# Optimization experiments

Hardware: AMD Instinct MI355X
Metric: run time of the kernel (lower is better)

## Reference

```python
import jax, jax.numpy as jnp
import numpy as np

INPUT_DIM = 512
N_CLASSES = 100
N_SUBNETS = 20
HIDDEN = 32
WS1 = INPUT_DIM * HIDDEN   # 16384
BS1 = HIDDEN               # 32
WS2 = HIDDEN * N_CLASSES   # 3200
BS2 = N_CLASSES            # 100
TOTAL = WS1 + BS1 + WS2 + BS2  # 19716
LN_EPS = 1e-5


def _layernorm(v, g, b):
    mu = jnp.mean(v, axis=-1, keepdims=True)
    var = jnp.mean(jnp.square(v - mu), axis=-1, keepdims=True)
    return (v - mu) * jax.lax.rsqrt(var + LN_EPS) * g + b


def setup_inputs() -> dict:
    key = jax.random.key(0)
    ks = jax.random.split(key, 12)
    def lin(k, fan_in, shape):
        bound = 1.0 / np.sqrt(fan_in)
        return jax.random.uniform(k, shape, jnp.float32, -bound, bound)
    return {
        "x": jax.random.normal(ks[0], (32768, INPUT_DIM), jnp.float32),
        "W_h1": lin(ks[1], INPUT_DIM, (128, INPUT_DIM)),
        "b_h1": lin(ks[2], INPUT_DIM, (128,)),
        "g1": jnp.ones((128,), jnp.float32),
        "be1": jnp.zeros((128,), jnp.float32),
        "W_h2": lin(ks[3], 128, (256, 128)),
        "b_h2": lin(ks[4], 128, (256,)),
        "g2": jnp.ones((256,), jnp.float32),
        "be2": jnp.zeros((256,), jnp.float32),
        "W_h3": lin(ks[5], 256, (N_SUBNETS * TOTAL, 256)),
        "b_h3": lin(ks[6], 256, (N_SUBNETS * TOTAL,)),
        "ens_w": jnp.full((N_SUBNETS,), 1.0 / N_SUBNETS, jnp.float32),
    }


def reference(x, W_h1, b_h1, g1, be1, W_h2, b_h2, g2, be2, W_h3, b_h3, ens_w):
    # context from support set (= x itself): (1, input_dim)
    context = jnp.mean(x, axis=0, keepdims=True)
    # hypernet MLP (eval mode: dropout = identity)
    h = jax.nn.relu(_layernorm(context @ W_h1.T + b_h1, g1, be1))
    h = jax.nn.relu(_layernorm(h @ W_h2.T + b_h2, g2, be2))
    all_params = (h @ W_h3.T + b_h3).reshape(N_SUBNETS, TOTAL)
    # split generated params (same layout as torch .view)
    W1 = all_params[:, :WS1].reshape(N_SUBNETS, HIDDEN, INPUT_DIM)       # (S,H,I)
    b1 = all_params[:, WS1:WS1 + BS1]                                     # (S,H)
    W2 = all_params[:, WS1 + BS1:WS1 + BS1 + WS2].reshape(N_SUBNETS, N_CLASSES, HIDDEN)  # (S,C,H)
    b2 = all_params[:, WS1 + BS1 + WS2:]                                  # (S,C)
    # batched per-subnet 2-layer nets (dropout p=0.2 is identity in eval)
    hh = jax.nn.relu(jnp.einsum('bi,shi->sbh', x, W1) + b1[:, None, :])   # (S,B,H)
    logits = jnp.einsum('sbh,sch->sbc', hh, W2) + b2[:, None, :]          # (S,B,C)
    w = jax.nn.softmax(ens_w)                                             # (S,)
    return jnp.einsum('s,sbc->bc', w, logits)                             # (B,C)
```

## Files before the change

kernel.cpp:

```cpp
#include <hip/hip_runtime.h>
#include <hip/hip_bf16.h>

#define BATCH   32768
#define DIM     512
#define H1N     128
#define H2N     256
#define NSUB    20
#define HID     32
#define NCLS    100
#define NHID    640
#define TOTALP  19716
#define NPAR    394320
#define WS1P    16384
#define WS1B1   16416
#define WS2END  19616

#define OFF_PART 0
#define OFF_H    262144
#define OFF_W    262400
#define OFF_B1   262432
#define OFF_B2R  263072
#define OFF_W1B  265072
#define OFF_W2B  428912

typedef __attribute__((ext_vector_type(8))) short short8;
typedef __attribute__((ext_vector_type(4))) float f32x4;

static __device__ inline unsigned short f2bf(float f) {
    __hip_bfloat16 h = __float2bfloat16(f);
    return *reinterpret_cast<unsigned short*>(&h);
}

static __device__ __forceinline__ void gload16(const void* g, void* l) {
    __builtin_amdgcn_global_load_lds(
        (const __attribute__((address_space(1))) void*)g,
        (__attribute__((address_space(3))) void*)l, 16, 0, 0);
}

__global__ __launch_bounds__(256) void k1_colsum(const float* __restrict__ x,
                                                 float* __restrict__ F) {
    __shared__ float sP[DIM];
    int t = threadIdx.x, bid = blockIdx.x;
    int par = t >> 7;
    int c4 = (t & 127) * 4;
    const float* xb = x + (size_t)bid * 64 * DIM;
    float4 acc = make_float4(0.f, 0.f, 0.f, 0.f);
    #pragma unroll 8
    for (int i = 0; i < 32; ++i) {
        int r = 2 * i + par;
        float4 v = *(const float4*)(xb + r * DIM + c4);
        acc.x += v.x; acc.y += v.y; acc.z += v.z; acc.w += v.w;
    }
    if (par == 0) *(float4*)(sP + c4) = acc;
    __syncthreads();
    if (par == 1) {
        float4 p = *(const float4*)(sP + c4);
        p.x += acc.x; p.y += acc.y; p.z += acc.z; p.w += acc.w;
        *(float4*)(F + OFF_PART + bid * DIM + c4) = p;
    }
}

__global__ __launch_bounds__(256) void k2_hyper(
    const float* __restrict__ Wh1, const float* __restrict__ bh1,
    const float* __restrict__ g1,  const float* __restrict__ be1,
    const float* __restrict__ Wh2, const float* __restrict__ bh2,
    const float* __restrict__ g2,  const float* __restrict__ be2,
    const float* __restrict__ ensw, float* __restrict__ F)
{
    __shared__ __align__(16) float sctx[DIM];
    __shared__ __align__(16) float sP2[DIM];
    __shared__ __align__(16) float sh1[H1N];
    __shared__ __align__(16) float sh2[H2N];
    int t = threadIdx.x;

    {
        int c4 = (t & 127) * 4;
        int half = t >> 7;
        float4 a = make_float4(0.f, 0.f, 0.f, 0.f);
        #pragma unroll 8
        for (int b = half * 256; b < half * 256 + 256; ++b) {
            float4 v = *(const float4*)(F + OFF_PART + b * DIM + c4);
            a.x += v.x; a.y += v.y; a.z += v.z; a.w += v.w;
        }
        if (half == 0) *(float4*)(sP2 + c4) = a;
        __syncthreads();
        if (half == 1) {
            float4 o = *(const float4*)(sP2 + c4);
            o.x = (o.x + a.x) * (1.0f / BATCH);
            o.y = (o.y + a.y) * (1.0f / BATCH);
            o.z = (o.z + a.z) * (1.0f / BATCH);
            o.w = (o.w + a.w) * (1.0f / BATCH);
            *(float4*)(sctx + c4) = o;
        }
        __syncthreads();
    }

    if (t < H1N) {
        float v = bh1[t];
        const float4* w = (const float4*)(Wh1 + t * DIM);
        for (int k = 0; k < DIM / 4; ++k) {
            float4 ww = w[k]; float4 c = *(const float4*)(sctx + k * 4);
            v += ww.x * c.x + ww.y * c.y + ww.z * c.z + ww.w * c.w;
        }
        sh1[t] = v;
    }
    __syncthreads();
    {
        float mu = 0.f;
        for (int k = 0; k < H1N; ++k) mu += sh1[k];
        mu *= (1.0f / H1N);
        float var = 0.f;
        for (int k = 0; k < H1N; ++k) { float d = sh1[k] - mu; var += d * d; }
        var *= (1.0f / H1N);
        float inv = rsqrtf(var + 1e-5f);
        __syncthreads();
        if (t < H1N) {
            float v = (sh1[t] - mu) * inv * g1[t] + be1[t];
            sh1[t] = fmaxf(v, 0.f);
        }
        __syncthreads();
    }

    {
        float v = bh2[t];
        const float4* w = (const float4*)(Wh2 + t * H1N);
        for (int k = 0; k < H1N / 4; ++k) {
            float4 ww = w[k]; float4 c = *(const float4*)(sh1 + k * 4);
            v += ww.x * c.x + ww.y * c.y + ww.z * c.z + ww.w * c.w;
        }
        sh2[t] = v;
    }
    __syncthreads();
    {
        float mu = 0.f;
        for (int k = 0; k < H2N; ++k) mu += sh2[k];
        mu *= (1.0f / H2N);
        float var = 0.f;
        for (int k = 0; k < H2N; ++k) { float d = sh2[k] - mu; var += d * d; }
        var *= (1.0f / H2N);
        float inv = rsqrtf(var + 1e-5f);
        float v = (sh2[t] - mu) * inv * g2[t] + be2[t];
        F[OFF_H + t] = fmaxf(v, 0.f);
    }

    if (t == 0) {
        float m = -1e30f;
        for (int s = 0; s < NSUB; ++s) m = fmaxf(m, ensw[s]);
        float sum = 0.f, e[NSUB];
        for (int s = 0; s < NSUB; ++s) { e[s] = __expf(ensw[s] - m); sum += e[s]; }
        for (int s = 0; s < NSUB; ++s) F[OFF_W + s] = e[s] / sum;
    }
}

static __device__ __forceinline__ void k3_pack(float* F, int row, float val) {
    __hip_bfloat16* W1B = (__hip_bfloat16*)(F + OFF_W1B);
    __hip_bfloat16* W2B = (__hip_bfloat16*)(F + OFF_W2B);
    int s = row / TOTALP;
    int r = row - s * TOTALP;
    if (r < WS1P) {
        int hh = r >> 9, k = r & 511;
        W1B[(s * HID + hh) * DIM + k] = __float2bfloat16(val);
    } else if (r < WS1B1) {
        F[OFF_B1 + s * HID + (r - WS1P)] = val;
    } else if (r < WS2END) {
        int q = r - WS1B1; int c = q >> 5, hh = q & 31;
        float ws = F[OFF_W + s];
        W2B[c * NHID + s * HID + hh] = __float2bfloat16(ws * val);
    } else {
        F[OFF_B2R + s * NCLS + (r - WS2END)] = val;
    }
}

__global__ __launch_bounds__(256) void k3_gemv(
    const float* __restrict__ Wh3, const float* __restrict__ bh3, float* __restrict__ F)
{
    int t = threadIdx.x;
    int wid = t >> 6, lane = t & 63;
    int row0 = blockIdx.x * 8 + wid * 2;
    const float4 h = *(const float4*)(F + OFF_H + lane * 4);
    const float4 w0 = *(const float4*)(Wh3 + (size_t)row0 * 256 + lane * 4);
    const float4 w1 = *(const float4*)(Wh3 + (size_t)(row0 + 1) * 256 + lane * 4);
    float d0 = w0.x * h.x + w0.y * h.y + w0.z * h.z + w0.w * h.w;
    float d1 = w1.x * h.x + w1.y * h.y + w1.z * h.z + w1.w * h.w;
    #pragma unroll
    for (int off = 32; off; off >>= 1) {
        d0 += __shfl_down(d0, off);
        d1 += __shfl_down(d1, off);
    }
    if (lane == 0) {
        k3_pack(F, row0,     d0 + bh3[row0]);
        k3_pack(F, row0 + 1, d1 + bh3[row0 + 1]);
    }
}

__global__ __launch_bounds__(256) void gemm_fused(
    const float* __restrict__ x, const __hip_bfloat16* __restrict__ W1B,
    const __hip_bfloat16* __restrict__ W2B, const float* __restrict__ F,
    float* __restrict__ out)
{
    __shared__ __align__(16) unsigned char sB[2][128 * 128];
    __shared__ __align__(16) unsigned char sP[64 * 256];
    const int t = threadIdx.x;
    int bid = blockIdx.x;
    const int cpx = gridDim.x >> 3;
    bid = (bid & 7) * cpx + (bid >> 3);
    const int Row0 = bid * 64;
    const int wid = t >> 6, lane = t & 63;
    const int l16 = lane & 15, lq = lane >> 4;

    f32x4 acc1[8], acc2[8];
    #pragma unroll
    for (int fn = 0; fn < 8; ++fn) acc2[fn] = (f32x4){0.f, 0.f, 0.f, 0.f};

    auto stageW1 = [&](int n1, int kc, int b) {
        #pragma unroll
        for (int i = 0; i < 4; ++i) {
            int cidx = wid * 4 + i;
            int ul = cidx * 64 + lane;
            int row = ul >> 3, u = ul & 7;
            gload16(W1B + (size_t)(n1 * 128 + row) * 512 + kc + ((u ^ (row & 7)) << 3),
                    &sB[b][cidx * 1024]);
        }
    };
    auto stageW2 = [&](int n1, int h, int b) {
        #pragma unroll
        for (int i = 0; i < 4; ++i) {
            int cidx = wid * 4 + i;
            int ul = cidx * 64 + lane;
            int row = ul >> 3, u = ul & 7;
            gload16(W2B + (size_t)row * NHID + n1 * 128 + h * 64 + ((u ^ (row & 7)) << 3),
                    &sB[b][cidx * 1024]);
        }
    };

    stageW1(0, 0, 0);

    short8 afr[16];
    {
        const float* xrow = x + (size_t)(Row0 + wid * 16 + l16) * 512;
        #pragma unroll
        for (int i = 0; i < 16; ++i) {
            int k0 = (i >> 1) * 64 + (i & 1) * 32 + lq * 8;
            float4 a = *(const float4*)(xrow + k0);
            float4 b = *(const float4*)(xrow + k0 + 4);
            unsigned int p[4];
            p[0] = (unsigned)f2bf(a.x) | ((unsigned)f2bf(a.y) << 16);
            p[1] = (unsigned)f2bf(a.z) | ((unsigned)f2bf(a.w) << 16);
            p[2] = (unsigned)f2bf(b.x) | ((unsigned)f2bf(b.y) << 16);
            p[3] = (unsigned)f2bf(b.z) | ((unsigned)f2bf(b.w) << 16);
            afr[i] = *(short8*)p;
        }
    }
    asm volatile("s_waitcnt vmcnt(0)" ::: "memory");
    __builtin_amdgcn_s_barrier();

    auto comp1 = [&](int st, int b) {
        #pragma unroll
        for (int kk = 0; kk < 2; ++kk) {
            int u = kk * 4 + lq;
            short8 af = afr[st * 2 + kk];
            short8 bfv[8];
            #pragma unroll
            for (int fn = 0; fn < 8; ++fn) {
                int rw = fn * 16 + l16;
                bfv[fn] = *(const short8*)(&sB[b][rw * 128 + ((u ^ (rw & 7)) << 4)]);
            }
            #pragma unroll
            for (int fn = 0; fn < 8; ++fn)
                acc1[fn] = __builtin_amdgcn_mfma_f32_16x16x32_bf16(
                    af, bfv[fn], acc1[fn], 0, 0, 0);
        }
    };
    auto comp2 = [&](int h, int b) {
        #pragma unroll
        for (int kk = 0; kk < 2; ++kk) {
            int u = kk * 4 + lq;
            int punit = (h * 2 + kk) * 4 + lq;
            int arow = wid * 16 + l16;
            short8 af = *(const short8*)(&sP[arow * 256 + ((punit ^ (arow & 7)) << 4)]);
            short8 bfv[8];
            #pragma unroll
            for (int fn = 0; fn < 8; ++fn) {
                int rw = fn * 16 + l16;
                bfv[fn] = *(const short8*)(&sB[b][rw * 128 + ((u ^ (rw & 7)) << 4)]);
            }
            #pragma unroll
            for (int fn = 0; fn < 8; ++fn)
                acc2[fn] = __builtin_amdgcn_mfma_f32_16x16x32_bf16(
                    af, bfv[fn], acc2[fn], 0, 0, 0);
        }
    };

    int buf = 0;
    float b1r[8];
    for (int n1 = 0; n1 < 5; ++n1) {
        #pragma unroll
        for (int st = 0; st < 10; ++st) {
            if (st < 9) {
                if (st + 1 < 8) stageW1(n1, (st + 1) * 64, buf ^ 1);
                else stageW2(n1, st + 1 - 8, buf ^ 1);
            } else if (n1 < 4) {
                stageW1(n1 + 1, 0, buf ^ 1);
            }
            if (st == 9 && n1 == 4)
                asm volatile("s_waitcnt vmcnt(0)" ::: "memory");
            else
                asm volatile("s_waitcnt vmcnt(4)" ::: "memory");
            __builtin_amdgcn_s_barrier();
            __builtin_amdgcn_sched_barrier(0);

            if (st == 0) {
                #pragma unroll
                for (int fn = 0; fn < 8; ++fn) {
                    acc1[fn] = (f32x4){0.f, 0.f, 0.f, 0.f};
                    b1r[fn] = F[OFF_B1 + n1 * 128 + fn * 16 + l16];
                }
            }
            if (st < 8) comp1(st, buf);
            else comp2(st - 8, buf);
            if (st == 7) {
                #pragma unroll
                for (int fn = 0; fn < 8; ++fn) {
                    int col = fn * 16 + l16;
                    int unit = col >> 3;
                    #pragma unroll
                    for (int r = 0; r < 4; ++r) {
                        int row = wid * 16 + lq * 4 + r;
                        float v = fmaxf(acc1[fn][r] + b1r[fn], 0.f);
                        *(unsigned short*)(&sP[row * 256 + ((unit ^ (row & 7)) << 4)
                                           + (col & 7) * 2]) = f2bf(v);
                    }
                }
            }
            __builtin_amdgcn_sched_barrier(0);
            __builtin_amdgcn_s_barrier();
            buf ^= 1;
        }
    }

    float* sBe = (float*)sP;
    if (t < 128) {
        float b = 0.f;
        if (t < NCLS) {
            #pragma unroll
            for (int s = 0; s < NSUB; ++s)
                b += F[OFF_W + s] * F[OFF_B2R + s * NCLS + t];
        }
        sBe[t] = b;
    }
    __syncthreads();

    #pragma unroll
    for (int fn = 0; fn < 8; ++fn) {
        int gcol = fn * 16 + l16;
        if (gcol < NCLS) {
            float be = sBe[gcol];
            #pragma unroll
            for (int r = 0; r < 4; ++r) {
                int grow = Row0 + wid * 16 + lq * 4 + r;
                out[(size_t)grow * NCLS + gcol] = acc2[fn][r] + be;
            }
        }
    }
}

extern "C" void kernel_launch(void* const* d_in, const int* in_sizes, int n_in,
                              void* d_out, int out_size, void* d_ws, size_t ws_size,
                              hipStream_t stream)
{
    const float* x    = (const float*)d_in[0];
    const float* Wh1  = (const float*)d_in[1];
    const float* bh1  = (const float*)d_in[2];
    const float* g1   = (const float*)d_in[3];
    const float* be1  = (const float*)d_in[4];
    const float* Wh2  = (const float*)d_in[5];
    const float* bh2  = (const float*)d_in[6];
    const float* g2   = (const float*)d_in[7];
    const float* be2  = (const float*)d_in[8];
    const float* Wh3  = (const float*)d_in[9];
    const float* bh3  = (const float*)d_in[10];
    const float* ensw = (const float*)d_in[11];
    float* F = (float*)d_ws;
    float* out = (float*)d_out;

    const __hip_bfloat16* W1B = (const __hip_bfloat16*)(F + OFF_W1B);
    const __hip_bfloat16* W2B = (const __hip_bfloat16*)(F + OFF_W2B);

    k1_colsum<<<512, 256, 0, stream>>>(x, F);
    k2_hyper<<<1, 256, 0, stream>>>(Wh1, bh1, g1, be1, Wh2, bh2, g2, be2, ensw, F);
    k3_gemv<<<NPAR / 8, 256, 0, stream>>>(Wh3, bh3, F);
    gemm_fused<<<BATCH / 64, 256, 0, stream>>>(x, W1B, W2B, F, out);
}
```

Baseline: 182.9 us.

## Retile fused GEMM warps as 2x2 and parallelize column-sum reduction

The fused MLP GEMM moves from four warps that each own 16 rows by all 128 columns to a 2x2 warp grid, where each warp owns 32 rows by 64 columns. This halves the B-fragment LDS reads per MFMA and adds a launch-bounds hint of two blocks per SM. A new 16-block kernel pre-reduces the 512 partial column sums into 8, so the single-block hypernet kernel no longer serially reads 512 rows. The A fragments in registers double and an extra kernel launch is added, which could raise register pressure and launch overhead.

```diff
diff --git a/kernel.cpp b/kernel.cpp
--- a/kernel.cpp
+++ b/kernel.cpp
@@ -22,6 +22,7 @@
 #define OFF_B2R  263072
 #define OFF_W1B  265072
 #define OFF_W2B  428912
+#define OFF_PRED 470000
 
 typedef __attribute__((ext_vector_type(8))) short short8;
 typedef __attribute__((ext_vector_type(4))) float f32x4;
@@ -60,6 +61,17 @@
     }
 }
 
+__global__ __launch_bounds__(256) void k1b_red(float* __restrict__ F) {
+    int bx = blockIdx.x;
+    int orow = bx >> 1;
+    int c = (bx & 1) * 256 + threadIdx.x;
+    float s = 0.f;
+    #pragma unroll 8
+    for (int j = 0; j < 64; ++j)
+        s += F[OFF_PART + (orow * 64 + j) * DIM + c];
+    F[OFF_PRED + orow * DIM + c] = s;
+}
+
 __global__ __launch_bounds__(256) void k2_hyper(
     const float* __restrict__ Wh1, const float* __restrict__ bh1,
     const float* __restrict__ g1,  const float* __restrict__ be1,
@@ -68,32 +80,23 @@
     const float* __restrict__ ensw, float* __restrict__ F)
 {
     __shared__ __align__(16) float sctx[DIM];
-    __shared__ __align__(16) float sP2[DIM];
     __shared__ __align__(16) float sh1[H1N];
     __shared__ __align__(16) float sh2[H2N];
     int t = threadIdx.x;
 
-    {
-        int c4 = (t & 127) * 4;
-        int half = t >> 7;
+    if (t < 128) {
+        int c4 = t * 4;
         float4 a = make_float4(0.f, 0.f, 0.f, 0.f);
-        #pragma unroll 8
-        for (int b = half * 256; b < half * 256 + 256; ++b) {
-            float4 v = *(const float4*)(F + OFF_PART + b * DIM + c4);
+        #pragma unroll
+        for (int b = 0; b < 8; ++b) {
+            float4 v = *(const float4*)(F + OFF_PRED + b * DIM + c4);
             a.x += v.x; a.y += v.y; a.z += v.z; a.w += v.w;
         }
-        if (half == 0) *(float4*)(sP2 + c4) = a;
-        __syncthreads();
-        if (half == 1) {
-            float4 o = *(const float4*)(sP2 + c4);
-            o.x = (o.x + a.x) * (1.0f / BATCH);
-            o.y = (o.y + a.y) * (1.0f / BATCH);
-            o.z = (o.z + a.z) * (1.0f / BATCH);
-            o.w = (o.w + a.w) * (1.0f / BATCH);
-            *(float4*)(sctx + c4) = o;
-        }
-        __syncthreads();
-    }
+        a.x *= (1.0f / BATCH); a.y *= (1.0f / BATCH);
+        a.z *= (1.0f / BATCH); a.w *= (1.0f / BATCH);
+        *(float4*)(sctx + c4) = a;
+    }
+    __syncthreads();
 
     if (t < H1N) {
         float v = bh1[t];
@@ -193,7 +196,7 @@
     }
 }
 
-__global__ __launch_bounds__(256) void gemm_fused(
+__global__ __launch_bounds__(256, 2) void gemm_fused(
     const float* __restrict__ x, const __hip_bfloat16* __restrict__ W1B,
     const __hip_bfloat16* __restrict__ W2B, const float* __restrict__ F,
     float* __restrict__ out)
@@ -207,10 +210,14 @@
     const int Row0 = bid * 64;
     const int wid = t >> 6, lane = t & 63;
     const int l16 = lane & 15, lq = lane >> 4;
-
-    f32x4 acc1[8], acc2[8];
+    const int wr = wid >> 1, wc = wid & 1;
+
+    f32x4 acc1[2][4], acc2[2][4];
     #pragma unroll
-    for (int fn = 0; fn < 8; ++fn) acc2[fn] = (f32x4){0.f, 0.f, 0.f, 0.f};
+    for (int fm = 0; fm < 2; ++fm)
+        #pragma unroll
+        for (int fn = 0; fn < 4; ++fn)
+            acc2[fm][fn] = (f32x4){0.f, 0.f, 0.f, 0.f};
 
     auto stageW1 = [&](int n1, int kc, int b) {
         #pragma unroll
@@ -235,9 +242,10 @@
 
     stageW1(0, 0, 0);
 
-    short8 afr[16];
-    {
-        const float* xrow = x + (size_t)(Row0 + wid * 16 + l16) * 512;
+    short8 afr[2][16];
+    #pragma unroll
+    for (int fm = 0; fm < 2; ++fm) {
+        const float* xrow = x + (size_t)(Row0 + wr * 32 + fm * 16 + l16) * 512;
         #pragma unroll
         for (int i = 0; i < 16; ++i) {
             int k0 = (i >> 1) * 64 + (i & 1) * 32 + lq * 8;
@@ -248,7 +256,7 @@
             p[1] = (unsigned)f2bf(a.z) | ((unsigned)f2bf(a.w) << 16);
             p[2] = (unsigned)f2bf(b.x) | ((unsigned)f2bf(b.y) << 16);
             p[3] = (unsigned)f2bf(b.z) | ((unsigned)f2bf(b.w) << 16);
-            afr[i] = *(short8*)p;
+            afr[fm][i] = *(short8*)p;
         }
     }
     asm volatile("s_waitcnt vmcnt(0)" ::: "memory");
@@ -258,17 +266,18 @@
         #pragma unroll
         for (int kk = 0; kk < 2; ++kk) {
             int u = kk * 4 + lq;
-            short8 af = afr[st * 2 + kk];
-            short8 bfv[8];
-            #pragma unroll
-            for (int fn = 0; fn < 8; ++fn) {
-                int rw = fn * 16 + l16;
+            short8 bfv[4];
+            #pragma unroll
+            for (int fn = 0; fn < 4; ++fn) {
+                int rw = wc * 64 + fn * 16 + l16;
                 bfv[fn] = *(const short8*)(&sB[b][rw * 128 + ((u ^ (rw & 7)) << 4)]);
             }
             #pragma unroll
-            for (int fn = 0; fn < 8; ++fn)
-                acc1[fn] = __builtin_amdgcn_mfma_f32_16x16x32_bf16(
-                    af, bfv[fn], acc1[fn], 0, 0, 0);
+            for (int fm = 0; fm < 2; ++fm)
+                #pragma unroll
+                for (int fn = 0; fn < 4; ++fn)
+                    acc1[fm][fn] = __builtin_amdgcn_mfma_f32_16x16x32_bf16(
+                        afr[fm][st * 2 + kk], bfv[fn], acc1[fm][fn], 0, 0, 0);
         }
     };
     auto comp2 = [&](int h, int b) {
@@ -276,23 +285,28 @@
         for (int kk = 0; kk < 2; ++kk) {
             int u = kk * 4 + lq;
             int punit = (h * 2 + kk) * 4 + lq;
-            int arow = wid * 16 + l16;
-            short8 af = *(const short8*)(&sP[arow * 256 + ((punit ^ (arow & 7)) << 4)]);
-            short8 bfv[8];
-            #pragma unroll
-            for (int fn = 0; fn < 8; ++fn) {
-                int rw = fn * 16 + l16;
+            short8 af[2], bfv[4];
+            #pragma unroll
+            for (int fm = 0; fm < 2; ++fm) {
+                int arow = wr * 32 + fm * 16 + l16;
+                af[fm] = *(const short8*)(&sP[arow * 256 + ((punit ^ (arow & 7)) << 4)]);
+            }
+            #pragma unroll
+            for (int fn = 0; fn < 4; ++fn) {
+                int rw = wc * 64 + fn * 16 + l16;
                 bfv[fn] = *(const short8*)(&sB[b][rw * 128 + ((u ^ (rw & 7)) << 4)]);
             }
             #pragma unroll
-            for (int fn = 0; fn < 8; ++fn)
-                acc2[fn] = __builtin_amdgcn_mfma_f32_16x16x32_bf16(
-                    af, bfv[fn], acc2[fn], 0, 0, 0);
+            for (int fm = 0; fm < 2; ++fm)
+                #pragma unroll
+                for (int fn = 0; fn < 4; ++fn)
+                    acc2[fm][fn] = __builtin_amdgcn_mfma_f32_16x16x32_bf16(
+                        af[fm], bfv[fn], acc2[fm][fn], 0, 0, 0);
         }
     };
 
     int buf = 0;
-    float b1r[8];
+    float b1r[4];
     for (int n1 = 0; n1 < 5; ++n1) {
         #pragma unroll
         for (int st = 0; st < 10; ++st) {
@@ -311,24 +325,30 @@
 
             if (st == 0) {
                 #pragma unroll
-                for (int fn = 0; fn < 8; ++fn) {
-                    acc1[fn] = (f32x4){0.f, 0.f, 0.f, 0.f};
-                    b1r[fn] = F[OFF_B1 + n1 * 128 + fn * 16 + l16];
-                }
+                for (int fm = 0; fm < 2; ++fm)
+                    #pragma unroll
+                    for (int fn = 0; fn < 4; ++fn)
+                        acc1[fm][fn] = (f32x4){0.f, 0.f, 0.f, 0.f};
+                #pragma unroll
+                for (int fn = 0; fn < 4; ++fn)
+                    b1r[fn] = F[OFF_B1 + n1 * 128 + wc * 64 + fn * 16 + l16];
             }
             if (st < 8) comp1(st, buf);
             else comp2(st - 8, buf);
             if (st == 7) {
                 #pragma unroll
-                for (int fn = 0; fn < 8; ++fn) {
-                    int col = fn * 16 + l16;
-                    int unit = col >> 3;
+                for (int fm = 0; fm < 2; ++fm) {
                     #pragma unroll
-                    for (int r = 0; r < 4; ++r) {
-                        int row = wid * 16 + lq * 4 + r;
-                        float v = fmaxf(acc1[fn][r] + b1r[fn], 0.f);
-                        *(unsigned short*)(&sP[row * 256 + ((unit ^ (row & 7)) << 4)
-                                           + (col & 7) * 2]) = f2bf(v);
+                    for (int fn = 0; fn < 4; ++fn) {
+                        int col = wc * 64 + fn * 16 + l16;
+                        int unit = col >> 3;
+                        #pragma unroll
+                        for (int r = 0; r < 4; ++r) {
+                            int row = wr * 32 + fm * 16 + lq * 4 + r;
+                            float v = fmaxf(acc1[fm][fn][r] + b1r[fn], 0.f);
+                            *(unsigned short*)(&sP[row * 256 + ((unit ^ (row & 7)) << 4)
+                                               + (col & 7) * 2]) = f2bf(v);
+                        }
                     }
                 }
             }
@@ -351,14 +371,17 @@
     __syncthreads();
 
     #pragma unroll
-    for (int fn = 0; fn < 8; ++fn) {
-        int gcol = fn * 16 + l16;
-        if (gcol < NCLS) {
-            float be = sBe[gcol];
-            #pragma unroll
-            for (int r = 0; r < 4; ++r) {
-                int grow = Row0 + wid * 16 + lq * 4 + r;
-                out[(size_t)grow * NCLS + gcol] = acc2[fn][r] + be;
+    for (int fm = 0; fm < 2; ++fm) {
+        #pragma unroll
+        for (int fn = 0; fn < 4; ++fn) {
+            int gcol = wc * 64 + fn * 16 + l16;
+            if (gcol < NCLS) {
+                float be = sBe[gcol];
+                #pragma unroll
+                for (int r = 0; r < 4; ++r) {
+                    int grow = Row0 + wr * 32 + fm * 16 + lq * 4 + r;
+                    out[(size_t)grow * NCLS + gcol] = acc2[fm][fn][r] + be;
+                }
             }
         }
     }
@@ -387,6 +410,7 @@
     const __hip_bfloat16* W2B = (const __hip_bfloat16*)(F + OFF_W2B);
 
     k1_colsum<<<512, 256, 0, stream>>>(x, F);
+    k1b_red<<<16, 256, 0, stream>>>(F);
     k2_hyper<<<1, 256, 0, stream>>>(Wh1, bh1, g1, be1, Wh2, bh2, g2, be2, ensw, F);
     k3_gemv<<<NPAR / 8, 256, 0, stream>>>(Wh3, bh3, F);
     gemm_fused<<<BATCH / 64, 256, 0, stream>>>(x, W1B, W2B, F, out);
```

New measurement: 193.6 us. 1.06x slower.
